# Optimization experiments

Measured on AMD Instinct MI355X. Metric: run time of the kernel, lower is better.

The kernel has to match this reference:

```python
import jax, jax.numpy as jnp
import numpy as np

N_SRC = 100000
N_TGT = 100000
E = 600000
IN_SRC = 256
IN_TGT = 256
OUT = 128
LEAKY_SLOPE = 0.2


def setup_inputs() -> dict:
    key = jax.random.key(0)
    k0, k1, k2, k3, k4, k5 = jax.random.split(key, 6)
    src = jax.random.normal(k0, (N_SRC, IN_SRC), dtype=jnp.float32)
    tgt = jax.random.normal(k1, (N_TGT, IN_TGT), dtype=jnp.float32)
    # Linear weights stored as [in, out] so forward is x @ W (same math as torch Linear)
    W_src = jax.random.normal(k2, (IN_SRC, OUT), dtype=jnp.float32) * 0.06
    W_tgt = jax.random.normal(k3, (IN_TGT, OUT), dtype=jnp.float32) * 0.06
    a = jax.random.normal(k4, (2 * OUT, 1), dtype=jnp.float32) * 0.1
    edge_index = jax.random.randint(k5, (2, E), 0, N_SRC, dtype=jnp.int64)
    return {"src": src, "tgt": tgt, "W_src": W_src, "W_tgt": W_tgt, "a": a,
            "edge_index": edge_index}


def reference(src, tgt, W_src, W_tgt, a, edge_index):
    out_dim = W_src.shape[1]
    n_src = src.shape[0]
    h_i = src @ W_src  # [N_src, out]
    h_j = tgt @ W_tgt  # [N_tgt, out]
    src_id = edge_index[0]
    tgt_id = edge_index[1]
    # cat([h_i[s], h_j[t]]) @ a == (h_i @ a[:out])[s] + (h_j @ a[out:])[t]
    score_i = h_i @ a[:out_dim, 0]  # [N_src]
    score_j = h_j @ a[out_dim:, 0]  # [N_tgt]
    e = jax.nn.leaky_relu(score_i[src_id] + score_j[tgt_id],
                          negative_slope=LEAKY_SLOPE)  # [E]
    e = jnp.clip(e, -30.0, 30.0)
    exp_e = jnp.exp(e)
    denom = jax.ops.segment_sum(exp_e, src_id, num_segments=n_src)  # [N_src]
    alpha = exp_e / (denom[src_id] + 1e-8)  # [E]  (dropout: eval mode -> identity)
    msg = h_j[tgt_id] * alpha[:, None]  # [E, out]
    out = jax.ops.segment_sum(msg, src_id, num_segments=n_src)  # [N_src, out]
    return jax.nn.elu(out)  # concat=True branch
```

## Files before the change

kernel.cpp:

```cpp
#include <hip/hip_runtime.h>
#include <hip/hip_bf16.h>
#include <math.h>

#define IN_DIM 256
#define OUT_DIM 128
#define LEAKY 0.2f

typedef __attribute__((ext_vector_type(8))) short bf16x8;
typedef __attribute__((ext_vector_type(4))) float f32x4;

__device__ __forceinline__ unsigned short f2bf(float f) {
    union { float f; unsigned int u; } v; v.f = f;
    unsigned int r = v.u + 0x7FFFu + ((v.u >> 16) & 1u);
    return (unsigned short)(r >> 16);
}
__device__ __forceinline__ float bf2f(unsigned int hi16) {
    union { unsigned int u; float f; } v; v.u = hi16 << 16;
    return v.f;
}

__global__ __launch_bounds__(256) void prep_kernel(
    const float* __restrict__ W_src, const float* __restrict__ W_tgt,
    const float* __restrict__ a, float* __restrict__ wcomb,
    unsigned short* __restrict__ Wswz, int4* __restrict__ counts4, int n4) {
    if (blockIdx.x >= 17) {
        int i = (blockIdx.x - 17) * 256 + threadIdx.x;
        if (i < n4) counts4[i] = make_int4(0, 0, 0, 0);
        return;
    }
    if (blockIdx.x == 16) {
        int i = threadIdx.x;
        float s = 0.f;
        #pragma unroll 4
        for (int k = 0; k < OUT_DIM; ++k) s += W_src[i * OUT_DIM + k] * a[k];
        wcomb[i] = s;
        return;
    }
    int idx = blockIdx.x * 256 + threadIdx.x;
    int l  = idx & 63;
    int fj = (idx >> 6) & 7;
    int kc = idx >> 9;
    int col = fj * 16 + (l & 15);
    int kb  = kc * 32 + (l >> 4) * 8;
    unsigned int u[4];
    #pragma unroll
    for (int p = 0; p < 4; ++p) {
        unsigned short e0 = f2bf(W_tgt[(size_t)(kb + 2 * p + 0) * OUT_DIM + col]);
        unsigned short e1 = f2bf(W_tgt[(size_t)(kb + 2 * p + 1) * OUT_DIM + col]);
        u[p] = (unsigned int)e0 | ((unsigned int)e1 << 16);
    }
    *(uint4*)(Wswz + (size_t)idx * 8) = make_uint4(u[0], u[1], u[2], u[3]);
}

__global__ __launch_bounds__(256) void gemv_hist_kernel(
    const float* __restrict__ X, const float* __restrict__ w,
    float* __restrict__ score, int M,
    const int* __restrict__ src_id, int* __restrict__ counts,
    int* __restrict__ rank, int E) {
    int bid = blockIdx.x;
    if (bid & 1) {
        int e = (bid >> 1) * 256 + threadIdx.x;
        if (e < E) rank[e] = atomicAdd(&counts[src_id[e]], 1);
        return;
    }
    int row = (bid >> 1) * 32 + (threadIdx.x >> 3);
    if (row >= M) return;
    int k = threadIdx.x & 7;
    const float4* R = (const float4*)(X + (size_t)row * IN_DIM);
    const float4* W4 = (const float4*)w;
    float s = 0.f;
    #pragma unroll
    for (int c = 0; c < 8; ++c) {
        float4 x = R[k + 8 * c];
        float4 wv = W4[k + 8 * c];
        s += x.x * wv.x + x.y * wv.y + x.z * wv.z + x.w * wv.w;
    }
    s += __shfl_xor(s, 1);
    s += __shfl_xor(s, 2);
    s += __shfl_xor(s, 4);
    if (k == 0) score[row] = s;
}

__global__ __launch_bounds__(256) void gemm_mfma_kernel(
    const float* __restrict__ A,
    const unsigned short* __restrict__ Wswz,
    const float* __restrict__ a_hi,
    unsigned short* __restrict__ Hb,
    float* __restrict__ score, int M) {
    __shared__ unsigned short As[64 * 256];
    int tid = threadIdx.x;
    int w = tid >> 6;
    int l = tid & 63;
    int bm = blockIdx.x * 64;

    int srow = tid >> 4;
    int kcol = (tid & 15) * 4;

    float aw[8];
    #pragma unroll
    for (int j = 0; j < 8; ++j) aw[j] = a_hi[j * 16 + (l & 15)];

    f32x4 acc[8];
    f32x4 zero = {0.f, 0.f, 0.f, 0.f};
    #pragma unroll
    for (int j = 0; j < 8; ++j) acc[j] = zero;

    float4 pre[16];
    #pragma unroll
    for (int p = 0; p < 4; ++p) {
        int grow = bm + srow + p * 16;
        const float* rp = A + (size_t)(grow < M ? grow : M - 1) * IN_DIM;
        bool ok = grow < M;
        #pragma unroll
        for (int c = 0; c < 4; ++c) {
            float4 v = *(const float4*)(rp + c * 64 + kcol);
            pre[p * 4 + c] = ok ? v : make_float4(0.f, 0.f, 0.f, 0.f);
        }
    }
    #pragma unroll
    for (int p = 0; p < 4; ++p) {
        int row = srow + p * 16;
        #pragma unroll
        for (int c = 0; c < 4; ++c) {
            float4 v = pre[p * 4 + c];
            unsigned int b0 = (unsigned int)f2bf(v.x) | ((unsigned int)f2bf(v.y) << 16);
            unsigned int b1 = (unsigned int)f2bf(v.z) | ((unsigned int)f2bf(v.w) << 16);
            unsigned int byteoff =
                (unsigned int)(row * 512 + (c * 64 + kcol) * 2) ^ ((row & 7) << 4);
            *(uint2*)((char*)As + byteoff) = make_uint2(b0, b1);
        }
    }
    __syncthreads();

    #pragma unroll
    for (int kc = 0; kc < 8; ++kc) {
        int row = w * 16 + (l & 15);
        unsigned int byteoff =
            (unsigned int)(row * 512 + kc * 64 + (l >> 4) * 16) ^ ((row & 7) << 4);
        bf16x8 af = *(const bf16x8*)((const char*)As + byteoff);
        #pragma unroll
        for (int j = 0; j < 8; ++j) {
            bf16x8 bfj = *(const bf16x8*)(Wswz + ((size_t)(kc * 8 + j) * 64 + l) * 8);
            acc[j] = __builtin_amdgcn_mfma_f32_16x16x32_bf16(af, bfj, acc[j], 0, 0, 0);
        }
    }
    #pragma unroll
    for (int r = 0; r < 4; ++r) {
        int row = bm + w * 16 + (l >> 4) * 4 + r;
        if (row < M) {
            float s = 0.f;
            #pragma unroll
            for (int j = 0; j < 8; ++j) {
                float v = acc[j][r];
                Hb[(size_t)row * OUT_DIM + j * 16 + (l & 15)] = f2bf(v);
                s += v * aw[j];
            }
            s += __shfl_xor(s, 1); s += __shfl_xor(s, 2);
            s += __shfl_xor(s, 4); s += __shfl_xor(s, 8);
            if ((l & 15) == 0) score[row] = s;
        }
    }
}

__global__ __launch_bounds__(256) void scan1_kernel(
    const int* __restrict__ counts, int* __restrict__ offs,
    int* __restrict__ blockSums, int n) {
    __shared__ int sd[256];
    int b = blockIdx.x, tid = threadIdx.x;
    int base = b * 1024 + tid * 4;
    int v0 = base + 0 < n ? counts[base + 0] : 0;
    int v1 = base + 1 < n ? counts[base + 1] : 0;
    int v2 = base + 2 < n ? counts[base + 2] : 0;
    int v3 = base + 3 < n ? counts[base + 3] : 0;
    int p1 = v0, p2 = v0 + v1, p3 = v0 + v1 + v2;
    int tsum = p3 + v3;
    sd[tid] = tsum;
    __syncthreads();
    #pragma unroll
    for (int off = 1; off < 256; off <<= 1) {
        int t = tid >= off ? sd[tid - off] : 0;
        __syncthreads();
        sd[tid] += t;
        __syncthreads();
    }
    int ex = sd[tid] - tsum;
    if (base + 0 < n) offs[base + 0] = ex;
    if (base + 1 < n) offs[base + 1] = ex + p1;
    if (base + 2 < n) offs[base + 2] = ex + p2;
    if (base + 3 < n) offs[base + 3] = ex + p3;
    if (tid == 255) blockSums[b] = sd[255];
}

__global__ __launch_bounds__(256) void scan2_kernel(
    const int* __restrict__ blockSums, int* __restrict__ blockOffs, int nb) {
    __shared__ int sd[256];
    int tid = threadIdx.x;
    int v = tid < nb ? blockSums[tid] : 0;
    sd[tid] = v;
    __syncthreads();
    #pragma unroll
    for (int off = 1; off < 256; off <<= 1) {
        int t = tid >= off ? sd[tid - off] : 0;
        __syncthreads();
        sd[tid] += t;
        __syncthreads();
    }
    blockOffs[tid] = sd[tid] - v;
}

__global__ __launch_bounds__(256) void scatter_fused_kernel(
    const int* __restrict__ src_id, const int* __restrict__ tgt_id,
    const float* __restrict__ score_i, const float* __restrict__ score_j,
    const int* __restrict__ offs, const int* __restrict__ blockOffs,
    const int* __restrict__ rank, uint2* __restrict__ pairs, int E) {
    int e = blockIdx.x * blockDim.x + threadIdx.x;
    if (e >= E) return;
    int s = src_id[e], t = tgt_id[e];
    float x = score_i[s] + score_j[t];
    x = x > 0.f ? x : LEAKY * x;
    x = fminf(30.f, fmaxf(-30.f, x));
    float ex = expf(x);
    int p = offs[s] + blockOffs[s >> 10] + rank[e];
    pairs[p] = make_uint2((unsigned int)t, __float_as_uint(ex));
}

__global__ __launch_bounds__(256) void agg_kernel(
    const uint2* __restrict__ pairs, const int* __restrict__ offs,
    const int* __restrict__ blockOffs, const unsigned short* __restrict__ hjb,
    float* __restrict__ out, int N, int E) {
    int node = (int)((blockIdx.x * (long long)blockDim.x + threadIdx.x) >> 6);
    if (node >= N) return;
    int lane = threadIdx.x & 63;
    int q  = lane >> 4;
    int cl = lane & 15;
    int beg = offs[node] + blockOffs[node >> 10];
    int end = (node + 1 < N) ? offs[node + 1] + blockOffs[(node + 1) >> 10] : E;
    int deg = end - beg;
    float den = 0.f;
    float acc[8];
    #pragma unroll
    for (int i = 0; i < 8; ++i) acc[i] = 0.f;

    int iters = (deg + 3) >> 2;
    for (int it = 0; it < iters; ++it) {
        int e = q + 4 * it;
        bool valid = e < deg;
        int idx = beg + (valid ? e : 0);
        uint2 tw = pairs[idx];
        int t = (int)tw.x;
        float wgt = valid ? __uint_as_float(tw.y) : 0.f;
        den += wgt;
        uint4 u = *(const uint4*)(hjb + (size_t)t * OUT_DIM + cl * 8);
        acc[0] += bf2f(u.x & 0xffffu) * wgt;
        acc[1] += bf2f(u.x >> 16) * wgt;
        acc[2] += bf2f(u.y & 0xffffu) * wgt;
        acc[3] += bf2f(u.y >> 16) * wgt;
        acc[4] += bf2f(u.z & 0xffffu) * wgt;
        acc[5] += bf2f(u.z >> 16) * wgt;
        acc[6] += bf2f(u.w & 0xffffu) * wgt;
        acc[7] += bf2f(u.w >> 16) * wgt;
    }
    den += __shfl_xor(den, 16);
    den += __shfl_xor(den, 32);
    float inv = 1.f / (den + 1e-8f);
    #pragma unroll
    for (int i = 0; i < 8; ++i) {
        acc[i] += __shfl_xor(acc[i], 16);
        acc[i] += __shfl_xor(acc[i], 32);
        acc[i] *= inv;
        acc[i] = acc[i] > 0.f ? acc[i] : expm1f(acc[i]);
    }
    if (lane < 16) {
        float4 v0 = make_float4(acc[0], acc[1], acc[2], acc[3]);
        float4 v1 = make_float4(acc[4], acc[5], acc[6], acc[7]);
        *(float4*)(out + (size_t)node * OUT_DIM + cl * 8) = v0;
        *(float4*)(out + (size_t)node * OUT_DIM + cl * 8 + 4) = v1;
    }
}

__global__ __launch_bounds__(256) void edge_pass1_kernel(
    const int* __restrict__ src_id, const int* __restrict__ tgt_id,
    const float* __restrict__ score_i, const float* __restrict__ score_j,
    float* __restrict__ exp_e, float* __restrict__ denom, int E) {
    int e = blockIdx.x * blockDim.x + threadIdx.x;
    if (e >= E) return;
    int s = src_id[e], t = tgt_id[e];
    float x = score_i[s] + score_j[t];
    x = x > 0.f ? x : LEAKY * x;
    x = fminf(30.f, fmaxf(-30.f, x));
    float ex = expf(x);
    exp_e[e] = ex;
    atomicAdd(&denom[s], ex);
}

__global__ __launch_bounds__(256) void edge_pass2_kernel(
    const int* __restrict__ src_id, const int* __restrict__ tgt_id,
    const unsigned short* __restrict__ hjb, const float* __restrict__ exp_e,
    const float* __restrict__ denom, float* __restrict__ out, int E) {
    int idx = blockIdx.x * blockDim.x + threadIdx.x;
    int e = idx >> 6;
    if (e >= E) return;
    int lane = idx & 63;
    int s = src_id[e], t = tgt_id[e];
    float alpha = exp_e[e] / (denom[s] + 1e-8f);
    unsigned int u = *(const unsigned int*)(hjb + (size_t)t * OUT_DIM + lane * 2);
    atomicAdd(out + (size_t)s * OUT_DIM + lane * 2 + 0, bf2f(u & 0xffffu) * alpha);
    atomicAdd(out + (size_t)s * OUT_DIM + lane * 2 + 1, bf2f(u >> 16) * alpha);
}

__global__ __launch_bounds__(256) void elu_kernel(float* __restrict__ out, int n4) {
    int i = blockIdx.x * blockDim.x + threadIdx.x;
    if (i >= n4) return;
    float4 v = ((float4*)out)[i];
    v.x = v.x > 0.f ? v.x : expm1f(v.x);
    v.y = v.y > 0.f ? v.y : expm1f(v.y);
    v.z = v.z > 0.f ? v.z : expm1f(v.z);
    v.w = v.w > 0.f ? v.w : expm1f(v.w);
    ((float4*)out)[i] = v;
}

extern "C" void kernel_launch(void* const* d_in, const int* in_sizes, int n_in,
                              void* d_out, int out_size, void* d_ws, size_t ws_size,
                              hipStream_t stream) {
    const float* src   = (const float*)d_in[0];
    const float* tgt   = (const float*)d_in[1];
    const float* W_src = (const float*)d_in[2];
    const float* W_tgt = (const float*)d_in[3];
    const float* a     = (const float*)d_in[4];
    const int*   edge  = (const int*)d_in[5];

    int N_src = in_sizes[0] / IN_DIM;
    int N_tgt = in_sizes[1] / IN_DIM;
    int E     = in_sizes[5] / 2;
    const int* src_id = edge;
    const int* tgt_id = edge + E;

    float* out = (float*)d_out;

    char* ws = (char*)d_ws;
    size_t off = 0;
    auto alloc = [&](size_t bytes) {
        void* p = ws + off;
        off += (bytes + 255) & ~(size_t)255;
        return p;
    };

    unsigned short* hjb  = (unsigned short*)alloc((size_t)N_tgt * OUT_DIM * 2);
    float* score_i = (float*)alloc((size_t)N_src * 4);
    float* score_j = (float*)alloc((size_t)N_tgt * 4);
    float* wcomb   = (float*)alloc(256 * 4);
    unsigned short* Wswz = (unsigned short*)alloc(4096 * 8 * 2);
    int*   counts    = (int*)alloc(((size_t)N_src + 3) / 4 * 16);
    int*   offs      = (int*)alloc((size_t)(N_src + 1) * 4);
    int*   blockSums = (int*)alloc(256 * 4);
    int*   blockOffs = (int*)alloc(256 * 4);
    float* denom     = (float*)alloc((size_t)N_src * 4);
    float* exp_e     = (float*)alloc((size_t)E * 4);
    size_t fb_need = off;
    int*   rank      = (int*)alloc((size_t)E * 4);
    uint2* pairs     = (uint2*)alloc((size_t)E * 8);
    size_t csr_need = off;
    (void)fb_need;

    bool use_csr = (ws_size >= csr_need);

    int n4 = (N_src + 3) / 4;
    int zblocks = (n4 + 255) / 256;
    prep_kernel<<<17 + zblocks, 256, 0, stream>>>(
        W_src, W_tgt, a, wcomb, Wswz, (int4*)counts, n4);

    if (use_csr) {
        int gemvBlocks = (N_src + 31) / 32;
        int histBlocks = (E + 255) / 256;
        int half = gemvBlocks > histBlocks ? gemvBlocks : histBlocks;
        gemv_hist_kernel<<<2 * half, 256, 0, stream>>>(
            src, wcomb, score_i, N_src, src_id, counts, rank, E);
        gemm_mfma_kernel<<<(N_tgt + 63) / 64, 256, 0, stream>>>(
            tgt, Wswz, a + OUT_DIM, hjb, score_j, N_tgt);
        int nb = (N_src + 1023) / 1024;
        scan1_kernel<<<nb, 256, 0, stream>>>(counts, offs, blockSums, N_src);
        scan2_kernel<<<1, 256, 0, stream>>>(blockSums, blockOffs, nb);
        scatter_fused_kernel<<<(E + 255) / 256, 256, 0, stream>>>(
            src_id, tgt_id, score_i, score_j, offs, blockOffs, rank, pairs, E);
        agg_kernel<<<(N_src + 3) / 4, 256, 0, stream>>>(
            pairs, offs, blockOffs, hjb, out, N_src, E);
    } else {
        int gemvBlocks = (N_src + 31) / 32;
        gemv_hist_kernel<<<2 * gemvBlocks, 256, 0, stream>>>(
            src, wcomb, score_i, N_src, src_id, counts, rank, 0);
        gemm_mfma_kernel<<<(N_tgt + 63) / 64, 256, 0, stream>>>(
            tgt, Wswz, a + OUT_DIM, hjb, score_j, N_tgt);
        hipMemsetAsync(out, 0, (size_t)N_src * OUT_DIM * sizeof(float), stream);
        hipMemsetAsync(denom, 0, (size_t)N_src * sizeof(float), stream);
        edge_pass1_kernel<<<(E + 255) / 256, 256, 0, stream>>>(
            src_id, tgt_id, score_i, score_j, exp_e, denom, E);
        edge_pass2_kernel<<<(int)(((long long)E * 64 + 255) / 256), 256, 0, stream>>>(
            src_id, tgt_id, hjb, exp_e, denom, out, E);
        elu_kernel<<<(N_src * OUT_DIM / 4 + 255) / 256, 256, 0, stream>>>(
            out, N_src * OUT_DIM / 4);
    }
}
```

Before: 152.3 us.

## Fuse source GEMV, histogram and target MFMA GEMM into one interleaved launch

Merges the source-score GEMV with rank histogram kernel and the target bf16 MFMA GEMM into a single phase1 kernel. Each group of nine blocks is split by block index into two GEMM tiles, four GEMV tiles and three histogram tiles. The aim is to drop one launch and the serialization gap between the two bandwidth-bound phases, letting their memory traffic overlap. The cost is that every block now reserves the GEMM's 32KB shared-memory tile, which can lower occupancy for the lightweight GEMV and histogram blocks. Also, in the non-CSR fallback path the histogram now writes rank, which may lie outside the workspace.

```diff
diff --git a/kernel.cpp b/kernel.cpp
--- a/kernel.cpp
+++ b/kernel.cpp
@@ -52,46 +52,53 @@
     *(uint4*)(Wswz + (size_t)idx * 8) = make_uint4(u[0], u[1], u[2], u[3]);
 }
 
-__global__ __launch_bounds__(256) void gemv_hist_kernel(
+__global__ __launch_bounds__(256) void phase1_kernel(
+    const float* __restrict__ A, const unsigned short* __restrict__ Wswz,
+    const float* __restrict__ a_hi, unsigned short* __restrict__ Hb,
+    float* __restrict__ score_j, int Mt, int G,
     const float* __restrict__ X, const float* __restrict__ w,
-    float* __restrict__ score, int M,
+    float* __restrict__ score_i, int Ms, int V,
     const int* __restrict__ src_id, int* __restrict__ counts,
-    int* __restrict__ rank, int E) {
-    int bid = blockIdx.x;
-    if (bid & 1) {
-        int e = (bid >> 1) * 256 + threadIdx.x;
+    int* __restrict__ rank, int E, int H) {
+    __shared__ unsigned short As[64 * 256];
+    int b = blockIdx.x;
+    int g = b / 9;
+    int r = b - g * 9;
+    int tid = threadIdx.x;
+
+    if (r == 2 || r == 6 || r == 8) {
+        int hb = g * 3 + (r == 6 ? 1 : (r == 8 ? 2 : 0));
+        if (hb >= H) return;
+        int e = hb * 256 + tid;
         if (e < E) rank[e] = atomicAdd(&counts[src_id[e]], 1);
         return;
     }
-    int row = (bid >> 1) * 32 + (threadIdx.x >> 3);
-    if (row >= M) return;
-    int k = threadIdx.x & 7;
-    const float4* R = (const float4*)(X + (size_t)row * IN_DIM);
-    const float4* W4 = (const float4*)w;
-    float s = 0.f;
-    #pragma unroll
-    for (int c = 0; c < 8; ++c) {
-        float4 x = R[k + 8 * c];
-        float4 wv = W4[k + 8 * c];
-        s += x.x * wv.x + x.y * wv.y + x.z * wv.z + x.w * wv.w;
-    }
-    s += __shfl_xor(s, 1);
-    s += __shfl_xor(s, 2);
-    s += __shfl_xor(s, 4);
-    if (k == 0) score[row] = s;
-}
-
-__global__ __launch_bounds__(256) void gemm_mfma_kernel(
-    const float* __restrict__ A,
-    const unsigned short* __restrict__ Wswz,
-    const float* __restrict__ a_hi,
-    unsigned short* __restrict__ Hb,
-    float* __restrict__ score, int M) {
-    __shared__ unsigned short As[64 * 256];
-    int tid = threadIdx.x;
-    int w = tid >> 6;
+    if (r != 0 && r != 4) {
+        int vb = g * 4 + (r == 3 ? 1 : (r == 5 ? 2 : (r == 7 ? 3 : 0)));
+        if (vb >= V) return;
+        int row = vb * 32 + (tid >> 3);
+        if (row >= Ms) return;
+        int k = tid & 7;
+        const float4* R = (const float4*)(X + (size_t)row * IN_DIM);
+        const float4* W4 = (const float4*)w;
+        float s = 0.f;
+        #pragma unroll
+        for (int c = 0; c < 8; ++c) {
+            float4 x = R[k + 8 * c];
+            float4 wv = W4[k + 8 * c];
+            s += x.x * wv.x + x.y * wv.y + x.z * wv.z + x.w * wv.w;
+        }
+        s += __shfl_xor(s, 1);
+        s += __shfl_xor(s, 2);
+        s += __shfl_xor(s, 4);
+        if (k == 0) score_i[row] = s;
+        return;
+    }
+    int gb = g * 2 + (r == 4 ? 1 : 0);
+    if (gb >= G) return;
+    int w4 = tid >> 6;
     int l = tid & 63;
-    int bm = blockIdx.x * 64;
+    int bm = gb * 64;
 
     int srow = tid >> 4;
     int kcol = (tid & 15) * 4;
@@ -109,8 +116,8 @@
     #pragma unroll
     for (int p = 0; p < 4; ++p) {
         int grow = bm + srow + p * 16;
-        const float* rp = A + (size_t)(grow < M ? grow : M - 1) * IN_DIM;
-        bool ok = grow < M;
+        const float* rp = A + (size_t)(grow < Mt ? grow : Mt - 1) * IN_DIM;
+        bool ok = grow < Mt;
         #pragma unroll
         for (int c = 0; c < 4; ++c) {
             float4 v = *(const float4*)(rp + c * 64 + kcol);
@@ -134,7 +141,7 @@
 
     #pragma unroll
     for (int kc = 0; kc < 8; ++kc) {
-        int row = w * 16 + (l & 15);
+        int row = w4 * 16 + (l & 15);
         unsigned int byteoff =
             (unsigned int)(row * 512 + kc * 64 + (l >> 4) * 16) ^ ((row & 7) << 4);
         bf16x8 af = *(const bf16x8*)((const char*)As + byteoff);
@@ -145,19 +152,19 @@
         }
     }
     #pragma unroll
-    for (int r = 0; r < 4; ++r) {
-        int row = bm + w * 16 + (l >> 4) * 4 + r;
-        if (row < M) {
+    for (int rr = 0; rr < 4; ++rr) {
+        int row = bm + w4 * 16 + (l >> 4) * 4 + rr;
+        if (row < Mt) {
             float s = 0.f;
             #pragma unroll
             for (int j = 0; j < 8; ++j) {
-                float v = acc[j][r];
+                float v = acc[j][rr];
                 Hb[(size_t)row * OUT_DIM + j * 16 + (l & 15)] = f2bf(v);
                 s += v * aw[j];
             }
             s += __shfl_xor(s, 1); s += __shfl_xor(s, 2);
             s += __shfl_xor(s, 4); s += __shfl_xor(s, 8);
-            if ((l & 15) == 0) score[row] = s;
+            if ((l & 15) == 0) score_j[row] = s;
         }
     }
 }
@@ -369,14 +376,20 @@
     prep_kernel<<<17 + zblocks, 256, 0, stream>>>(
         W_src, W_tgt, a, wcomb, Wswz, (int4*)counts, n4);
 
+    int G = (N_tgt + 63) / 64;
+    int V = (N_src + 31) / 32;
+    int H = (E + 255) / 256;
+    int gmax = (G + 1) / 2;
+    int vmax = (V + 3) / 4;
+    int hmax = (H + 2) / 3;
+    int groups = gmax > vmax ? gmax : vmax;
+    if (hmax > groups) groups = hmax;
+    phase1_kernel<<<groups * 9, 256, 0, stream>>>(
+        tgt, Wswz, a + OUT_DIM, hjb, score_j, N_tgt, G,
+        src, wcomb, score_i, N_src, V,
+        src_id, counts, rank, E, H);
+
     if (use_csr) {
-        int gemvBlocks = (N_src + 31) / 32;
-        int histBlocks = (E + 255) / 256;
-        int half = gemvBlocks > histBlocks ? gemvBlocks : histBlocks;
-        gemv_hist_kernel<<<2 * half, 256, 0, stream>>>(
-            src, wcomb, score_i, N_src, src_id, counts, rank, E);
-        gemm_mfma_kernel<<<(N_tgt + 63) / 64, 256, 0, stream>>>(
-            tgt, Wswz, a + OUT_DIM, hjb, score_j, N_tgt);
         int nb = (N_src + 1023) / 1024;
         scan1_kernel<<<nb, 256, 0, stream>>>(counts, offs, blockSums, N_src);
         scan2_kernel<<<1, 256, 0, stream>>>(blockSums, blockOffs, nb);
@@ -385,11 +398,6 @@
         agg_kernel<<<(N_src + 3) / 4, 256, 0, stream>>>(
             pairs, offs, blockOffs, hjb, out, N_src, E);
     } else {
-        int gemvBlocks = (N_src + 31) / 32;
-        gemv_hist_kernel<<<2 * gemvBlocks, 256, 0, stream>>>(
-            src, wcomb, score_i, N_src, src_id, counts, rank, 0);
-        gemm_mfma_kernel<<<(N_tgt + 63) / 64, 256, 0, stream>>>(
-            tgt, Wswz, a + OUT_DIM, hjb, score_j, N_tgt);
         hipMemsetAsync(out, 0, (size_t)N_src * OUT_DIM * sizeof(float), stream);
         hipMemsetAsync(denom, 0, (size_t)N_src * sizeof(float), stream);
         edge_pass1_kernel<<<(E + 255) / 256, 256, 0, stream>>>(
```

Measured after the change: 142.1 us. 1.07x faster.

## Stage GEMM over K chunks and cache swizzled weights in LDS

Applied to the files above, without the earlier changes.

The MFMA GEMM kernel now walks K in four chunks of 64. For each chunk it loads an A slice and the matching slice of swizzled bf16 weights, writes both into shared memory, and feeds the MFMAs from LDS rather than reading weights straight from global memory per wave. This shrinks the A tile in LDS from 32KB to 8KB (plus 16KB for B), which could allow more resident blocks, and it stops every wave from re-reading weights through global memory. In exchange it adds a barrier per chunk and shortens the prefetch depth, so load latency may be exposed.

```diff
diff --git a/kernel.cpp b/kernel.cpp
--- a/kernel.cpp
+++ b/kernel.cpp
@@ -87,9 +87,10 @@
     const float* __restrict__ a_hi,
     unsigned short* __restrict__ Hb,
     float* __restrict__ score, int M) {
-    __shared__ unsigned short As[64 * 256];
+    __shared__ unsigned short As[64 * 64];
+    __shared__ bf16x8 Bs[1024];
     int tid = threadIdx.x;
-    int w = tid >> 6;
+    int w4 = tid >> 6;
     int l = tid & 63;
     int bm = blockIdx.x * 64;
 
@@ -105,53 +106,58 @@
     #pragma unroll
     for (int j = 0; j < 8; ++j) acc[j] = zero;
 
-    float4 pre[16];
-    #pragma unroll
-    for (int p = 0; p < 4; ++p) {
-        int grow = bm + srow + p * 16;
-        const float* rp = A + (size_t)(grow < M ? grow : M - 1) * IN_DIM;
-        bool ok = grow < M;
+    #pragma unroll
+    for (int q = 0; q < 4; ++q) {
+        float4 preA[4];
         #pragma unroll
-        for (int c = 0; c < 4; ++c) {
-            float4 v = *(const float4*)(rp + c * 64 + kcol);
-            pre[p * 4 + c] = ok ? v : make_float4(0.f, 0.f, 0.f, 0.f);
+        for (int p = 0; p < 4; ++p) {
+            int grow = bm + srow + p * 16;
+            const float* rp = A + (size_t)(grow < M ? grow : M - 1) * IN_DIM + q * 64;
+            float4 v = *(const float4*)(rp + kcol);
+            preA[p] = (grow < M) ? v : make_float4(0.f, 0.f, 0.f, 0.f);
         }
-    }
-    #pragma unroll
-    for (int p = 0; p < 4; ++p) {
-        int row = srow + p * 16;
+        uint4 preB[4];
         #pragma unroll
-        for (int c = 0; c < 4; ++c) {
-            float4 v = pre[p * 4 + c];
+        for (int c = 0; c < 4; ++c)
+            preB[c] = *(const uint4*)(Wswz + ((size_t)q * 1024 + tid * 4 + c) * 8);
+
+        if (q) __syncthreads();
+        #pragma unroll
+        for (int p = 0; p < 4; ++p) {
+            int row = srow + p * 16;
+            float4 v = preA[p];
             unsigned int b0 = (unsigned int)f2bf(v.x) | ((unsigned int)f2bf(v.y) << 16);
             unsigned int b1 = (unsigned int)f2bf(v.z) | ((unsigned int)f2bf(v.w) << 16);
             unsigned int byteoff =
-                (unsigned int)(row * 512 + (c * 64 + kcol) * 2) ^ ((row & 7) << 4);
+                (unsigned int)(row * 128 + kcol * 2) ^ ((row & 7) << 4);
             *(uint2*)((char*)As + byteoff) = make_uint2(b0, b1);
         }
-    }
-    __syncthreads();
-
-    #pragma unroll
-    for (int kc = 0; kc < 8; ++kc) {
-        int row = w * 16 + (l & 15);
-        unsigned int byteoff =
-            (unsigned int)(row * 512 + kc * 64 + (l >> 4) * 16) ^ ((row & 7) << 4);
-        bf16x8 af = *(const bf16x8*)((const char*)As + byteoff);
         #pragma unroll
-        for (int j = 0; j < 8; ++j) {
-            bf16x8 bfj = *(const bf16x8*)(Wswz + ((size_t)(kc * 8 + j) * 64 + l) * 8);
-            acc[j] = __builtin_amdgcn_mfma_f32_16x16x32_bf16(af, bfj, acc[j], 0, 0, 0);
+        for (int c = 0; c < 4; ++c)
+            *(uint4*)&Bs[tid * 4 + c] = preB[c];
+        __syncthreads();
+
+        #pragma unroll
+        for (int kcl = 0; kcl < 2; ++kcl) {
+            int row = w4 * 16 + (l & 15);
+            unsigned int byteoff =
+                (unsigned int)(row * 128 + kcl * 64 + (l >> 4) * 16) ^ ((row & 7) << 4);
+            bf16x8 af = *(const bf16x8*)((const char*)As + byteoff);
+            #pragma unroll
+            for (int j = 0; j < 8; ++j) {
+                bf16x8 bfj = Bs[(kcl * 8 + j) * 64 + l];
+                acc[j] = __builtin_amdgcn_mfma_f32_16x16x32_bf16(af, bfj, acc[j], 0, 0, 0);
+            }
         }
     }
     #pragma unroll
-    for (int r = 0; r < 4; ++r) {
-        int row = bm + w * 16 + (l >> 4) * 4 + r;
+    for (int rr = 0; rr < 4; ++rr) {
+        int row = bm + w4 * 16 + (l >> 4) * 4 + rr;
         if (row < M) {
             float s = 0.f;
             #pragma unroll
             for (int j = 0; j < 8; ++j) {
-                float v = acc[j][r];
+                float v = acc[j][rr];
                 Hb[(size_t)row * OUT_DIM + j * 16 + (l & 15)] = f2bf(v);
                 s += v * aw[j];
             }
```

Measured after the change: 173.5 us. 13.9% more time.
